# Optimization experiments

Measured on AMD Instinct MI355X. Metric: run time of the kernel, lower is better.

Reference implementation:

```python
import jax, jax.numpy as jnp
import numpy as np

B, T, S, V, D, H = 32, 50, 40, 32000, 512, 1024


def setup_inputs() -> dict:
    key = jax.random.key(0)
    ks = jax.random.split(key, 14)
    s_ih = 1.0 / np.sqrt(H)
    return {
        "zh_gruths": jax.random.randint(ks[0], (B, T), 0, V),
        "encoder_hs": jax.random.normal(ks[1], (B, S, H), jnp.float32),
        "encoder_h_n": jax.random.normal(ks[2], (1, B, H), jnp.float32) * 0.1,
        "encoder_c_n": jax.random.normal(ks[3], (1, B, H), jnp.float32) * 0.1,
        "entext_len": jax.random.randint(ks[4], (B,), 1, S + 1),
        "teacher_forcing_ratio": 1,
        "emb": jax.random.normal(ks[5], (V, D), jnp.float32) * 0.02,
        "W_ih": jax.random.normal(ks[6], (4 * H, D), jnp.float32) * s_ih,
        "W_hh": jax.random.normal(ks[7], (4 * H, H), jnp.float32) * s_ih,
        "b_ih": jax.random.normal(ks[8], (4 * H,), jnp.float32) * s_ih,
        "b_hh": jax.random.normal(ks[9], (4 * H,), jnp.float32) * s_ih,
        "W_ht": jax.random.normal(ks[10], (H, 2 * H), jnp.float32) * (1.0 / np.sqrt(2 * H)),
        "b_ht": jnp.zeros((H,), jnp.float32),
        "W_voc": jax.random.normal(ks[11], (V, H), jnp.float32) * s_ih,
        "b_voc": jnp.zeros((V,), jnp.float32),
    }


def reference(zh_gruths, encoder_hs, encoder_h_n, encoder_c_n, entext_len,
              teacher_forcing_ratio, emb, W_ih, W_hh, b_ih, b_hh,
              W_ht, b_ht, W_voc, b_voc):
    # teacher_forcing_ratio == 1 -> always teacher forcing (deterministic branch)
    xs = jnp.swapaxes(emb[zh_gruths], 0, 1)  # [T, B, D]
    hx0, cx0 = encoder_h_n[0], encoder_c_n[0]  # [B, H]

    def step(carry, xt):
        hx, cx = carry
        gates = xt @ W_ih.T + b_ih + hx @ W_hh.T + b_hh  # [B, 4H]
        i, f, g, o = jnp.split(gates, 4, axis=-1)  # torch gate order i,f,g,o
        i, f, o = jax.nn.sigmoid(i), jax.nn.sigmoid(f), jax.nn.sigmoid(o)
        cx = f * cx + i * jnp.tanh(g)
        hx = o * jnp.tanh(cx)
        # dot attention over encoder states
        scores = jnp.einsum('bsh,bh->bs', encoder_hs, hx)
        attn = jax.nn.softmax(scores, axis=-1)
        ctx = jnp.einsum('bs,bsh->bh', attn, encoder_hs)
        hx_atten = jnp.tanh(jnp.concatenate([ctx, hx], axis=-1) @ W_ht.T + b_ht)
        logits_t = hx_atten @ W_voc.T + b_voc  # [B, V]
        return (hx, cx), logits_t

    _, logits = jax.lax.scan(step, (hx0, cx0), xs)  # [T, B, V]
    logits = jnp.swapaxes(logits, 0, 1)  # [B, T, V]
    predicts = jnp.argmax(logits, axis=-1)  # [B, T]
    return logits, predicts
```

## Files before the change

### kernel.cpp

```cpp
#include <hip/hip_runtime.h>
#include <math.h>

typedef short bf16x8 __attribute__((ext_vector_type(8)));
typedef float f32x4 __attribute__((ext_vector_type(4)));
typedef float f32x2 __attribute__((ext_vector_type(2)));
typedef unsigned int uint;
typedef uint u32x4 __attribute__((ext_vector_type(4)));
typedef unsigned long long ull;
typedef unsigned short ushort;

#define Bz 32
#define Tz 50
#define Sz 40
#define Vz 32000
#define Dz 512
#define Hz 1024
#define Mz 1600
#define Mp 1664
#define NWG_REC 96

__device__ __forceinline__ float bf2f(ushort h) {
    uint u = ((uint)h) << 16;
    return __builtin_bit_cast(float, u);
}
__device__ __forceinline__ void splitf(float f, ushort& hi, ushort& lo) {
    uint u = __builtin_bit_cast(uint, f);
    hi = (ushort)(u >> 16);
    float rem = f - __builtin_bit_cast(float, u & 0xFFFF0000u);
    lo = (ushort)(__builtin_bit_cast(uint, rem) >> 16);
}
__device__ __forceinline__ float sigf(float x) { return 1.f / (1.f + expf(-x)); }

__device__ __forceinline__ uint ld_sc1(const uint* p) {
    uint v;
    asm volatile("global_load_dword %0, %1, off sc0 sc1\n\ts_waitcnt vmcnt(0)"
                 : "=&v"(v) : "v"(p) : "memory");
    return v;
}
__device__ __forceinline__ void st_sc1(uint* p, uint v) {
    asm volatile("global_store_dword %0, %1, off sc0 sc1" :: "v"(p), "v"(v) : "memory");
}

__global__ __launch_bounds__(256) void k_pre(ushort* hxA_hi, ushort* hxA_lo, float* cx,
                                             ushort* AH_hi, ushort* AH_lo, uint* flags,
                                             const float* h0, const float* c0) {
    int gid = blockIdx.x * 256 + threadIdx.x;
    if (gid < 32768) {
        float v = h0[gid];
        ushort hi, lo;
        splitf(v, hi, lo);
        hxA_hi[gid] = hi;
        hxA_lo[gid] = lo;
    } else if (gid < 65536) {
        cx[gid - 32768] = c0[gid - 32768];
    } else if (gid < 196608) {
        int g = gid - 65536;
        AH_hi[(long)Mz * 2048 + g] = 0;
        AH_lo[(long)Mz * 2048 + g] = 0;
    } else if (gid < 196608 + 2048) {
        st_sc1(&flags[gid - 196608], 0u);
    }
}

__global__ __launch_bounds__(256) void k_wsplit(const float* __restrict__ src,
                                                ushort* __restrict__ hi, ushort* __restrict__ lo,
                                                int n4) {
    int stride = gridDim.x * 256;
    for (int i = blockIdx.x * 256 + threadIdx.x; i < n4; i += stride) {
        float4 f = *(const float4*)(src + (long)i * 4);
        float vv[4] = {f.x, f.y, f.z, f.w};
        ushort h[4], l[4];
#pragma unroll
        for (int e = 0; e < 4; ++e) splitf(vv[e], h[e], l[e]);
        uint2 hp, lp;
        hp.x = (uint)h[0] | ((uint)h[1] << 16);
        hp.y = (uint)h[2] | ((uint)h[3] << 16);
        lp.x = (uint)l[0] | ((uint)l[1] << 16);
        lp.y = (uint)l[2] | ((uint)l[3] << 16);
        *(uint2*)(hi + (long)i * 4) = hp;
        *(uint2*)(lo + (long)i * 4) = lp;
    }
}

__global__ __launch_bounds__(256, 1) void k_xgemm(const float* __restrict__ emb,
                                                  const int* __restrict__ tok,
                                                  const float* __restrict__ Wih,
                                                  const float* __restrict__ bih,
                                                  const float* __restrict__ bhh,
                                                  float* __restrict__ gx) {
    __shared__ ushort sAh[128][40];
    __shared__ ushort sAl[128][40];
    __shared__ ushort sBh[128][40];
    __shared__ ushort sBl[128][40];
    int bid = blockIdx.x;
    int mt = bid >> 5, nt = bid & 31;
    int tid = threadIdx.x;
    int row = tid >> 1, half = tid & 1;
    int wv = tid >> 6, lane = tid & 63;
    int wr = wv >> 1, wc = wv & 1;
    int m0 = wr * 64, n0 = wc * 64;
    int r16 = lane & 15, kg = lane >> 4, k0 = kg * 8;

    f32x4 acc[4][4];
#pragma unroll
    for (int i = 0; i < 4; i++)
#pragma unroll
        for (int j = 0; j < 4; j++) acc[i][j] = (f32x4){0.f, 0.f, 0.f, 0.f};

    int r = mt * 128 + row;
    int tk = (r < Mz) ? tok[r] : 0;
    const float* arow = emb + (long)tk * Dz;
    const float* brow = Wih + (long)(nt * 128 + row) * Dz;

    for (int kb = 0; kb < Dz; kb += 32) {
        {
            ushort hh[16], ll[16];
#pragma unroll
            for (int q = 0; q < 16; q += 4) {
                float4 w4 = (r < Mz) ? *(const float4*)(arow + kb + half * 16 + q)
                                     : (float4){0.f, 0.f, 0.f, 0.f};
                float vv[4] = {w4.x, w4.y, w4.z, w4.w};
#pragma unroll
                for (int e = 0; e < 4; ++e) splitf(vv[e], hh[q + e], ll[q + e]);
            }
            *(uint4*)&sAh[row][half * 16]     = *(uint4*)&hh[0];
            *(uint4*)&sAh[row][half * 16 + 8] = *(uint4*)&hh[8];
            *(uint4*)&sAl[row][half * 16]     = *(uint4*)&ll[0];
            *(uint4*)&sAl[row][half * 16 + 8] = *(uint4*)&ll[8];
        }
        {
            ushort hh[16], ll[16];
#pragma unroll
            for (int q = 0; q < 16; q += 4) {
                float4 w4 = *(const float4*)(brow + kb + half * 16 + q);
                float vv[4] = {w4.x, w4.y, w4.z, w4.w};
#pragma unroll
                for (int e = 0; e < 4; ++e) splitf(vv[e], hh[q + e], ll[q + e]);
            }
            *(uint4*)&sBh[row][half * 16]     = *(uint4*)&hh[0];
            *(uint4*)&sBh[row][half * 16 + 8] = *(uint4*)&hh[8];
            *(uint4*)&sBl[row][half * 16]     = *(uint4*)&ll[0];
            *(uint4*)&sBl[row][half * 16 + 8] = *(uint4*)&ll[8];
        }
        __syncthreads();
        bf16x8 af[4], alf[4], bhf[4], blf[4];
#pragma unroll
        for (int i = 0; i < 4; ++i) {
            af[i]  = *(const bf16x8*)&sAh[m0 + i * 16 + r16][k0];
            alf[i] = *(const bf16x8*)&sAl[m0 + i * 16 + r16][k0];
            bhf[i] = *(const bf16x8*)&sBh[n0 + i * 16 + r16][k0];
            blf[i] = *(const bf16x8*)&sBl[n0 + i * 16 + r16][k0];
        }
#pragma unroll
        for (int i = 0; i < 4; ++i)
#pragma unroll
            for (int jn = 0; jn < 4; ++jn) {
                acc[i][jn] = __builtin_amdgcn_mfma_f32_16x16x32_bf16(af[i],  bhf[jn], acc[i][jn], 0, 0, 0);
                acc[i][jn] = __builtin_amdgcn_mfma_f32_16x16x32_bf16(af[i],  blf[jn], acc[i][jn], 0, 0, 0);
                acc[i][jn] = __builtin_amdgcn_mfma_f32_16x16x32_bf16(alf[i], bhf[jn], acc[i][jn], 0, 0, 0);
            }
        __syncthreads();
    }
#pragma unroll
    for (int i = 0; i < 4; ++i) {
        int gr0 = mt * 128 + m0 + i * 16 + kg * 4;
#pragma unroll
        for (int reg = 0; reg < 4; ++reg) {
            int gr = gr0 + reg;
            if (gr >= Mz) continue;
#pragma unroll
            for (int jn = 0; jn < 4; ++jn) {
                int gc = nt * 128 + n0 + jn * 16 + r16;
                gx[(long)gr * 4096 + gc] = acc[i][jn][reg] + bih[gc] + bhh[gc];
            }
        }
    }
}

__global__ __launch_bounds__(512, 1) void k_recfused4(
    const float* __restrict__ gx,
    const ushort* __restrict__ Whi, const ushort* __restrict__ Wlo,
    ushort* __restrict__ hxA_hi, ushort* __restrict__ hxA_lo,
    float* __restrict__ hxh, float* __restrict__ cx,
    const float* __restrict__ enc,
    ushort* __restrict__ AH_hi, ushort* __restrict__ AH_lo,
    uint* flags) {
    __shared__ u32x4 stg4[8192];
    __shared__ float hxs[Hz];
    __shared__ float sc[64];
    __shared__ float aw[64];
    int wid = blockIdx.x, tid = threadIdx.x;
    uint* release = flags + 1024;

    for (int t = 0; t <= Tz; ++t) {
        if (wid < 64) {
            if (t < Tz) {
                int w = wid;
                int p = t & 1, q = p ^ 1;
                int ks = tid & 127;
                int r0 = tid >> 7;
                const ushort* planes[2] = { hxA_hi + p * 32768, hxA_lo + p * 32768 };
#pragma unroll
                for (int plane = 0; plane < 2; ++plane) {
                    const ushort* b0 = planes[plane] + r0 * 1024 + ks * 8;
                    u32x4 d0, d1, d2, d3, d4, d5, d6, d7;
                    asm volatile(
                        "global_load_dwordx4 %0, %8, off sc0 sc1\n\t"
                        "global_load_dwordx4 %1, %9, off sc0 sc1\n\t"
                        "global_load_dwordx4 %2, %10, off sc0 sc1\n\t"
                        "global_load_dwordx4 %3, %11, off sc0 sc1\n\t"
                        "global_load_dwordx4 %4, %12, off sc0 sc1\n\t"
                        "global_load_dwordx4 %5, %13, off sc0 sc1\n\t"
                        "global_load_dwordx4 %6, %14, off sc0 sc1\n\t"
                        "global_load_dwordx4 %7, %15, off sc0 sc1\n\t"
                        "s_waitcnt vmcnt(0)"
                        : "=&v"(d0), "=&v"(d1), "=&v"(d2), "=&v"(d3),
                          "=&v"(d4), "=&v"(d5), "=&v"(d6), "=&v"(d7)
                        : "v"(b0), "v"(b0 + 4096), "v"(b0 + 8192), "v"(b0 + 12288),
                          "v"(b0 + 16384), "v"(b0 + 20480), "v"(b0 + 24576), "v"(b0 + 28672)
                        : "memory");
                    int li = plane * 4096 + ks * 32;
                    stg4[li + ((r0 +  0 + ks) & 31)] = d0;
                    stg4[li + ((r0 +  4 + ks) & 31)] = d1;
                    stg4[li + ((r0 +  8 + ks) & 31)] = d2;
                    stg4[li + ((r0 + 12 + ks) & 31)] = d3;
                    stg4[li + ((r0 + 16 + ks) & 31)] = d4;
                    stg4[li + ((r0 + 20 + ks) & 31)] = d5;
                    stg4[li + ((r0 + 24 + ks) & 31)] = d6;
                    stg4[li + ((r0 + 28 + ks) & 31)] = d7;
                }
                __syncthreads();
                int kh = tid >> 6, lane = tid & 63;
                int r16 = lane & 15, kg = lane >> 4;
                int jbase = w * 16 + r16;
                const ushort* whbase = Whi + (long)jbase * 1024;
                const ushort* wlbase = Wlo + (long)jbase * 1024;
                f32x4 acc[2][4];
#pragma unroll
                for (int i = 0; i < 2; ++i)
#pragma unroll
                    for (int v = 0; v < 4; ++v) acc[i][v] = (f32x4){0.f, 0.f, 0.f, 0.f};
#pragma unroll
                for (int it = 0; it < 4; ++it) {
                    int ksl = kh * 16 + it * 4 + kg;
                    int k0 = ksl * 8;
                    bf16x8 a_h0 = *(const bf16x8*)&stg4[       ksl * 32 + ((r16 + ksl) & 31)];
                    bf16x8 a_l0 = *(const bf16x8*)&stg4[4096 + ksl * 32 + ((r16 + ksl) & 31)];
                    bf16x8 a_h1 = *(const bf16x8*)&stg4[       ksl * 32 + ((16 + r16 + ksl) & 31)];
                    bf16x8 a_l1 = *(const bf16x8*)&stg4[4096 + ksl * 32 + ((16 + r16 + ksl) & 31)];
                    bf16x8 bh[4], bl[4];
#pragma unroll
                    for (int v = 0; v < 4; ++v) {
                        bh[v] = *(const bf16x8*)(whbase + ((long)v << 20) + k0);
                        bl[v] = *(const bf16x8*)(wlbase + ((long)v << 20) + k0);
                    }
#pragma unroll
                    for (int v = 0; v < 4; ++v) {
                        acc[0][v] = __builtin_amdgcn_mfma_f32_16x16x32_bf16(a_h0, bh[v], acc[0][v], 0, 0, 0);
                        acc[0][v] = __builtin_amdgcn_mfma_f32_16x16x32_bf16(a_l0, bh[v], acc[0][v], 0, 0, 0);
                        acc[0][v] = __builtin_amdgcn_mfma_f32_16x16x32_bf16(a_h0, bl[v], acc[0][v], 0, 0, 0);
                        acc[1][v] = __builtin_amdgcn_mfma_f32_16x16x32_bf16(a_h1, bh[v], acc[1][v], 0, 0, 0);
                        acc[1][v] = __builtin_amdgcn_mfma_f32_16x16x32_bf16(a_l1, bh[v], acc[1][v], 0, 0, 0);
                        acc[1][v] = __builtin_amdgcn_mfma_f32_16x16x32_bf16(a_h1, bl[v], acc[1][v], 0, 0, 0);
                    }
                }
                __syncthreads();
                float* sgp = (float*)stg4;
#pragma unroll
                for (int i = 0; i < 2; ++i)
#pragma unroll
                    for (int v = 0; v < 4; ++v)
#pragma unroll
                        for (int reg = 0; reg < 4; ++reg)
                            sgp[(((kh * 4 + v) * 32) + i * 16 + kg * 4 + reg) * 16 + r16] = acc[i][v][reg];
                __syncthreads();
                int b = tid >> 4, h16 = tid & 15;
                int hg = w * 16 + h16;
                const float* gxr = gx + ((long)b * Tz + t) * 4096 + hg;
                float g0 = 0.f, g1 = 0.f, g2 = 0.f, g3 = 0.f;
#pragma unroll
                for (int khh = 0; khh < 8; ++khh) {
                    g0 += sgp[((khh * 4 + 0) * 32 + b) * 16 + h16];
                    g1 += sgp[((khh * 4 + 1) * 32 + b) * 16 + h16];
                    g2 += sgp[((khh * 4 + 2) * 32 + b) * 16 + h16];
                    g3 += sgp[((khh * 4 + 3) * 32 + b) * 16 + h16];
                }
                g0 += gxr[0]; g1 += gxr[1024]; g2 += gxr[2048]; g3 += gxr[3072];
                long ci = (long)b * Hz + hg;
                float c = sigf(g1) * cx[ci] + sigf(g0) * tanhf(g2);
                float hv = sigf(g3) * tanhf(c);
                cx[ci] = c;
                float* hp = hxh + ((long)t * Bz + b) * Hz + hg;
                asm volatile("global_store_dword %0, %1, off sc0 sc1" :: "v"(hp), "v"(hv));
                ushort hi, lo;
                splitf(hv, hi, lo);
                ushort* hip = hxA_hi + q * 32768 + ci;
                ushort* lop = hxA_lo + q * 32768 + ci;
                asm volatile("global_store_short %0, %1, off sc0 sc1" :: "v"(hip), "v"((uint)hi));
                asm volatile("global_store_short %0, %1, off sc0 sc1" :: "v"(lop), "v"((uint)lo));

                asm volatile("s_waitcnt vmcnt(0)" ::: "memory");
                __syncthreads();
                uint tgt = (uint)(t + 1);
                if (wid == 0) {
                    if (tid == 0) {
                        st_sc1(&flags[0], tgt);
                        asm volatile("s_waitcnt vmcnt(0)" ::: "memory");
                    }
                    if (tid < 64) {
                        while (ld_sc1(&flags[tid * 16]) < tgt) __builtin_amdgcn_s_sleep(1);
                    }
                    __syncthreads();
                    if (tid == 0) st_sc1(release, tgt);
                } else {
                    if (tid == 0) {
                        st_sc1(&flags[wid * 16], tgt);
                        while (ld_sc1(release) < tgt) __builtin_amdgcn_s_sleep(1);
                    }
                    __syncthreads();
                }
            }
        } else {
            if (t > 0) {
                int b = wid - 64, tt = t - 1;
                if (tid == 0) {
                    while (ld_sc1(release) < (uint)t) __builtin_amdgcn_s_sleep(1);
                }
                __syncthreads();
                const float* hsrc = hxh + ((long)tt * Bz + b) * Hz + tid * 2;
                f32x2 h2;
                asm volatile("global_load_dwordx2 %0, %1, off sc0 sc1\n\ts_waitcnt vmcnt(0)"
                             : "=&v"(h2) : "v"(hsrc) : "memory");
                hxs[tid * 2] = h2[0];
                hxs[tid * 2 + 1] = h2[1];
                __syncthreads();
                int wv = tid >> 6, lane = tid & 63;
                float hreg[16];
#pragma unroll
                for (int u = 0; u < 16; ++u) hreg[u] = hxs[lane * 16 + u];
                const float* eb = enc + (long)b * Sz * Hz;
                for (int s = wv; s < Sz; s += 8) {
                    const float* er = eb + (long)s * Hz + lane * 16;
                    float sum = 0.f;
#pragma unroll
                    for (int qq = 0; qq < 4; ++qq) {
                        float4 e4 = *(const float4*)(er + qq * 4);
                        sum += e4.x * hreg[qq*4] + e4.y * hreg[qq*4+1] + e4.z * hreg[qq*4+2] + e4.w * hreg[qq*4+3];
                    }
#pragma unroll
                    for (int off = 32; off >= 1; off >>= 1) sum += __shfl_xor(sum, off);
                    if (lane == 0) sc[s] = sum;
                }
                __syncthreads();
                if (tid < 64) {
                    float vv = (tid < Sz) ? sc[tid] : -3.402823e38f;
                    float mx = vv;
#pragma unroll
                    for (int off = 32; off >= 1; off >>= 1) mx = fmaxf(mx, __shfl_xor(mx, off));
                    float e = (tid < Sz) ? expf(vv - mx) : 0.f;
                    float ssum = e;
#pragma unroll
                    for (int off = 32; off >= 1; off >>= 1) ssum += __shfl_xor(ssum, off);
                    if (tid < Sz) aw[tid] = e / ssum;
                }
                __syncthreads();
                float c0 = 0.f, c1 = 0.f;
#pragma unroll 4
                for (int s = 0; s < Sz; ++s) {
                    float2 e2 = *(const float2*)(eb + (long)s * Hz + tid * 2);
                    float a = aw[s];
                    c0 += a * e2.x; c1 += a * e2.y;
                }
                long rr = (long)b * Tz + tt;
                ushort* dh = AH_hi + rr * 2048;
                ushort* dl = AH_lo + rr * 2048;
                ushort hi, lo;
                splitf(c0, hi, lo); dh[tid * 2]     = hi; dl[tid * 2]     = lo;
                splitf(c1, hi, lo); dh[tid * 2 + 1] = hi; dl[tid * 2 + 1] = lo;
                splitf(hxs[tid * 2],     hi, lo); dh[1024 + tid * 2]     = hi; dl[1024 + tid * 2]     = lo;
                splitf(hxs[tid * 2 + 1], hi, lo); dh[1024 + tid * 2 + 1] = hi; dl[1024 + tid * 2 + 1] = lo;
            }
        }
    }
}

__global__ __launch_bounds__(256, 1) void k_ht(const ushort* __restrict__ Ah,
                                               const ushort* __restrict__ Al,
                                               const ushort* __restrict__ Bh,
                                               const ushort* __restrict__ Bl,
                                               const float* __restrict__ bht,
                                               ushort* __restrict__ Hh, ushort* __restrict__ Hl) {
    __shared__ ushort sAh[128][40];
    __shared__ ushort sAl[128][40];
    __shared__ ushort sBh[128][40];
    __shared__ ushort sBl[128][40];
    int bid = blockIdx.x;
    int mt = bid >> 3, nt = bid & 7;
    int tid = threadIdx.x;
    int row = tid >> 1, half = tid & 1;
    int wv = tid >> 6, lane = tid & 63;
    int wr = wv >> 1, wc = wv & 1;
    int m0 = wr * 64, n0 = wc * 64;
    int r16 = lane & 15, kg = lane >> 4, k0 = kg * 8;

    f32x4 acc[4][4];
#pragma unroll
    for (int i = 0; i < 4; i++)
#pragma unroll
        for (int j = 0; j < 4; j++) acc[i][j] = (f32x4){0.f, 0.f, 0.f, 0.f};

    long arow = (long)(mt * 128 + row) * 2048;
    long brow = (long)(nt * 128 + row) * 2048;

    for (int kb = 0; kb < 2048; kb += 32) {
        const ushort* pa = Ah + arow + kb + half * 16;
        *(uint4*)&sAh[row][half * 16]     = *(const uint4*)pa;
        *(uint4*)&sAh[row][half * 16 + 8] = *(const uint4*)(pa + 8);
        const ushort* pl = Al + arow + kb + half * 16;
        *(uint4*)&sAl[row][half * 16]     = *(const uint4*)pl;
        *(uint4*)&sAl[row][half * 16 + 8] = *(const uint4*)(pl + 8);
        const ushort* pb = Bh + brow + kb + half * 16;
        *(uint4*)&sBh[row][half * 16]     = *(const uint4*)pb;
        *(uint4*)&sBh[row][half * 16 + 8] = *(const uint4*)(pb + 8);
        const ushort* pc = Bl + brow + kb + half * 16;
        *(uint4*)&sBl[row][half * 16]     = *(const uint4*)pc;
        *(uint4*)&sBl[row][half * 16 + 8] = *(const uint4*)(pc + 8);
        __syncthreads();
        bf16x8 af[4], alf[4], bhf[4], blf[4];
#pragma unroll
        for (int i = 0; i < 4; ++i) {
            af[i]  = *(const bf16x8*)&sAh[m0 + i * 16 + r16][k0];
            alf[i] = *(const bf16x8*)&sAl[m0 + i * 16 + r16][k0];
            bhf[i] = *(const bf16x8*)&sBh[n0 + i * 16 + r16][k0];
            blf[i] = *(const bf16x8*)&sBl[n0 + i * 16 + r16][k0];
        }
#pragma unroll
        for (int i = 0; i < 4; ++i)
#pragma unroll
            for (int jn = 0; jn < 4; ++jn) {
                acc[i][jn] = __builtin_amdgcn_mfma_f32_16x16x32_bf16(af[i],  bhf[jn], acc[i][jn], 0, 0, 0);
                acc[i][jn] = __builtin_amdgcn_mfma_f32_16x16x32_bf16(af[i],  blf[jn], acc[i][jn], 0, 0, 0);
                acc[i][jn] = __builtin_amdgcn_mfma_f32_16x16x32_bf16(alf[i], bhf[jn], acc[i][jn], 0, 0, 0);
            }
        __syncthreads();
    }
#pragma unroll
    for (int i = 0; i < 4; ++i) {
        int gr0 = mt * 128 + m0 + i * 16 + kg * 4;
#pragma unroll
        for (int reg = 0; reg < 4; ++reg) {
            int gr = gr0 + reg;
            bool valid = gr < Mz;
#pragma unroll
            for (int jn = 0; jn < 4; ++jn) {
                int gc = nt * 128 + n0 + jn * 16 + r16;
                float vv = tanhf(acc[i][jn][reg] + bht[gc]);
                ushort hi = 0, lo = 0;
                if (valid) splitf(vv, hi, lo);
                Hh[(long)gr * Hz + gc] = hi;
                Hl[(long)gr * Hz + gc] = lo;
            }
        }
    }
}

__global__ __launch_bounds__(256, 1) void k_voc3(
    const ushort* __restrict__ Ah, const ushort* __restrict__ Al,
    const ushort* __restrict__ Wh, const ushort* __restrict__ Wl,
    const float* __restrict__ bvoc,
    float* __restrict__ out, ull* __restrict__ keys) {
    __shared__ ushort sAh[128][40];
    __shared__ ushort sAl[128][40];
    __shared__ ushort sBh[128][40];
    __shared__ ushort sBl[128][40];
    int bid = blockIdx.x;
    int nt = bid % 250, mg = bid / 250;
    int mt_beg = (mg == 0) ? 0 : 7;
    int mt_end = (mg == 0) ? 7 : 13;
    int tid = threadIdx.x;
    int row = tid >> 1, half = tid & 1;
    int wv = tid >> 6, lane = tid & 63;
    int wr = wv >> 1, wc = wv & 1;
    int m0 = wr * 64, n0 = wc * 64;
    int r16 = lane & 15, kg = lane >> 4, k0 = kg * 8;

    long wrow = (long)(nt * 128 + row) * Hz;
    int vcol_base = nt * 128 + n0;

    for (int mt = mt_beg; mt < mt_end; ++mt) {
        f32x4 acc[4][4];
#pragma unroll
        for (int i = 0; i < 4; i++)
#pragma unroll
            for (int j = 0; j < 4; j++) acc[i][j] = (f32x4){0.f, 0.f, 0.f, 0.f};

        long arow = (long)(mt * 128 + row) * Hz;

        for (int kb = 0; kb < Hz; kb += 32) {
            const ushort* pa = Ah + arow + kb + half * 16;
            *(uint4*)&sAh[row][half * 16]     = *(const uint4*)pa;
            *(uint4*)&sAh[row][half * 16 + 8] = *(const uint4*)(pa + 8);
            const ushort* pl = Al + arow + kb + half * 16;
            *(uint4*)&sAl[row][half * 16]     = *(const uint4*)pl;
            *(uint4*)&sAl[row][half * 16 + 8] = *(const uint4*)(pl + 8);
            const ushort* pb = Wh + wrow + kb + half * 16;
            *(uint4*)&sBh[row][half * 16]     = *(const uint4*)pb;
            *(uint4*)&sBh[row][half * 16 + 8] = *(const uint4*)(pb + 8);
            const ushort* pc = Wl + wrow + kb + half * 16;
            *(uint4*)&sBl[row][half * 16]     = *(const uint4*)pc;
            *(uint4*)&sBl[row][half * 16 + 8] = *(const uint4*)(pc + 8);
            __syncthreads();
            bf16x8 af[4], alf[4], bhf[4], blf[4];
#pragma unroll
            for (int i = 0; i < 4; ++i) {
                af[i]  = *(const bf16x8*)&sAh[m0 + i * 16 + r16][k0];
                alf[i] = *(const bf16x8*)&sAl[m0 + i * 16 + r16][k0];
                bhf[i] = *(const bf16x8*)&sBh[n0 + i * 16 + r16][k0];
                blf[i] = *(const bf16x8*)&sBl[n0 + i * 16 + r16][k0];
            }
#pragma unroll
            for (int i = 0; i < 4; ++i)
#pragma unroll
                for (int jn = 0; jn < 4; ++jn) {
                    acc[i][jn] = __builtin_amdgcn_mfma_f32_16x16x32_bf16(af[i],  bhf[jn], acc[i][jn], 0, 0, 0);
                    acc[i][jn] = __builtin_amdgcn_mfma_f32_16x16x32_bf16(af[i],  blf[jn], acc[i][jn], 0, 0, 0);
                    acc[i][jn] = __builtin_amdgcn_mfma_f32_16x16x32_bf16(alf[i], bhf[jn], acc[i][jn], 0, 0, 0);
                }
            __syncthreads();
        }
#pragma unroll
        for (int i = 0; i < 4; ++i) {
            int gr0 = mt * 128 + m0 + i * 16 + kg * 4;
#pragma unroll
            for (int reg = 0; reg < 4; ++reg) {
                int gr = gr0 + reg;
                bool valid = gr < Mz;
                float bestv = -3.402823e38f;
                int bestc = 0;
#pragma unroll
                for (int jn = 0; jn < 4; ++jn) {
                    int gc = vcol_base + jn * 16 + r16;
                    float v = acc[i][jn][reg] + bvoc[gc];
                    if (valid) __builtin_nontemporal_store(v, &out[(long)gr * Vz + gc]);
                    if (v > bestv) { bestv = v; bestc = gc; }
                }
#pragma unroll
                for (int off = 1; off < 16; off <<= 1) {
                    float ov = __shfl_xor(bestv, off);
                    int oc = __shfl_xor(bestc, off);
                    if (ov > bestv || (ov == bestv && oc < bestc)) { bestv = ov; bestc = oc; }
                }
                if (valid && r16 == 0) {
                    uint u = __builtin_bit_cast(uint, bestv);
                    u = (u & 0x80000000u) ? ~u : (u | 0x80000000u);
                    keys[(long)gr * 512 + nt * 2 + wc] = (((ull)u) << 32) | (ull)(65535 - bestc);
                }
            }
        }
    }
}

__global__ __launch_bounds__(256) void k_argmax2(const ull* __restrict__ keys, float* __restrict__ pred) {
    int r = blockIdx.x, tid = threadIdx.x;
    ull best = 0;
    for (int j = tid; j < 500; j += 256) {
        ull k = keys[(long)r * 512 + j];
        if (k > best) best = k;
    }
    __shared__ ull sk[256];
    sk[tid] = best;
    __syncthreads();
    for (int s = 128; s > 0; s >>= 1) {
        if (tid < s) { if (sk[tid + s] > sk[tid]) sk[tid] = sk[tid + s]; }
        __syncthreads();
    }
    if (tid == 0) pred[r] = (float)(65535 - (int)(sk[0] & 0xFFFFull));
}

extern "C" void kernel_launch(void* const* d_in, const int* in_sizes, int n_in,
                              void* d_out, int out_size, void* d_ws, size_t ws_size,
                              hipStream_t stream) {
    const int*   tok  = (const int*)d_in[0];
    const float* enc  = (const float*)d_in[1];
    const float* h0   = (const float*)d_in[2];
    const float* c0   = (const float*)d_in[3];
    const float* emb  = (const float*)d_in[6];
    const float* Wih  = (const float*)d_in[7];
    const float* Whh  = (const float*)d_in[8];
    const float* bih  = (const float*)d_in[9];
    const float* bhh  = (const float*)d_in[10];
    const float* Wht  = (const float*)d_in[11];
    const float* bht  = (const float*)d_in[12];
    const float* Wvoc = (const float*)d_in[13];
    const float* bvoc = (const float*)d_in[14];
    float* out = (float*)d_out;

    char* base = (char*)d_ws;
    size_t off = 0;
    float*  gx      = (float*)(base + off);  off += (size_t)Mz * 4096 * 4;
    ushort* hxA_hi  = (ushort*)(base + off); off += 2 * 32768 * 2;
    ushort* hxA_lo  = (ushort*)(base + off); off += 2 * 32768 * 2;
    float*  cx      = (float*)(base + off);  off += 32768 * 4;
    float*  hxh     = (float*)(base + off);  off += (size_t)Tz * Bz * Hz * 4;
    ushort* AH_hi   = (ushort*)(base + off); off += (size_t)Mp * 2048 * 2;
    ushort* AH_lo   = (ushort*)(base + off); off += (size_t)Mp * 2048 * 2;
    ushort* Whh_hi  = (ushort*)(base + off); off += (size_t)4096 * 1024 * 2;
    ushort* Whh_lo  = (ushort*)(base + off); off += (size_t)4096 * 1024 * 2;
    ushort* Wht_hi  = (ushort*)(base + off); off += (size_t)1024 * 2048 * 2;
    ushort* Wht_lo  = (ushort*)(base + off); off += (size_t)1024 * 2048 * 2;
    ushort* Wvoc_hi = (ushort*)base;
    ushort* Wvoc_lo = Wvoc_hi + (size_t)Vz * Hz;
    size_t off2 = (size_t)Vz * Hz * 2 * 2;
    ushort* HXA_hi  = (ushort*)(base + off2); off2 += (size_t)Mp * 1024 * 2;
    ushort* HXA_lo  = (ushort*)(base + off2); off2 += (size_t)Mp * 1024 * 2;
    ull*    keys    = (ull*)(base + off2);    off2 += (size_t)Mz * 512 * 8;
    uint*   flags   = (uint*)(base + off2);   off2 += 8192;

    k_pre<<<776, 256, 0, stream>>>(hxA_hi, hxA_lo, cx, AH_hi, AH_lo, flags, h0, c0);
    k_wsplit<<<1024, 256, 0, stream>>>(Whh, Whh_hi, Whh_lo, 4096 * 1024 / 4);
    k_wsplit<<<512, 256, 0, stream>>>(Wht, Wht_hi, Wht_lo, 1024 * 2048 / 4);
    k_xgemm<<<13 * 32, 256, 0, stream>>>(emb, tok, Wih, bih, bhh, gx);

    k_recfused4<<<NWG_REC, 512, 0, stream>>>(gx, Whh_hi, Whh_lo, hxA_hi, hxA_lo, hxh, cx,
                                             enc, AH_hi, AH_lo, flags);

    k_ht<<<13 * 8, 256, 0, stream>>>(AH_hi, AH_lo, Wht_hi, Wht_lo, bht, HXA_hi, HXA_lo);
    k_wsplit<<<2048, 256, 0, stream>>>(Wvoc, Wvoc_hi, Wvoc_lo, Vz * Hz / 4);
    k_voc3<<<500, 256, 0, stream>>>(HXA_hi, HXA_lo, Wvoc_hi, Wvoc_lo, bvoc, out, keys);
    k_argmax2<<<Mz, 256, 0, stream>>>(keys, out + (long)Mz * Vz);
}
```

Before: 1.171 ms.

## Overlap vocab weight split with recurrence and replace central barrier with per-wave flag polling

New measurement: 1.136 ms. 3.0% less time.

```diff
diff --git a/kernel.cpp b/kernel.cpp
--- a/kernel.cpp
+++ b/kernel.cpp
@@ -17,7 +17,6 @@
 #define Hz 1024
 #define Mz 1600
 #define Mp 1664
-#define NWG_REC 96
 
 __device__ __forceinline__ float bf2f(ushort h) {
     uint u = ((uint)h) << 16;
@@ -177,32 +176,65 @@
     }
 }
 
-__global__ __launch_bounds__(512, 1) void k_recfused4(
+__global__ __launch_bounds__(512, 1) void k_recfused5(
     const float* __restrict__ gx,
     const ushort* __restrict__ Whi, const ushort* __restrict__ Wlo,
     ushort* __restrict__ hxA_hi, ushort* __restrict__ hxA_lo,
     float* __restrict__ hxh, float* __restrict__ cx,
     const float* __restrict__ enc,
     ushort* __restrict__ AH_hi, ushort* __restrict__ AH_lo,
-    uint* flags) {
+    uint* flags,
+    const float* __restrict__ Wvoc, ushort* __restrict__ Wvh, ushort* __restrict__ Wvl,
+    int do_wsplit) {
     __shared__ u32x4 stg4[8192];
     __shared__ float hxs[Hz];
     __shared__ float sc[64];
     __shared__ float aw[64];
     int wid = blockIdx.x, tid = threadIdx.x;
-    uint* release = flags + 1024;
+
+    if (wid >= 96) {
+        if (do_wsplit) {
+            int n4 = Vz * Hz / 4;
+            int stride = 160 * 512;
+            for (int i = (wid - 96) * 512 + tid; i < n4; i += stride) {
+                float4 f = *(const float4*)(Wvoc + (long)i * 4);
+                float vv[4] = {f.x, f.y, f.z, f.w};
+                ushort h[4], l[4];
+#pragma unroll
+                for (int e = 0; e < 4; ++e) splitf(vv[e], h[e], l[e]);
+                uint2 hp, lp;
+                hp.x = (uint)h[0] | ((uint)h[1] << 16);
+                hp.y = (uint)h[2] | ((uint)h[3] << 16);
+                lp.x = (uint)l[0] | ((uint)l[1] << 16);
+                lp.y = (uint)l[2] | ((uint)l[3] << 16);
+                *(uint2*)(Wvh + (long)i * 4) = hp;
+                *(uint2*)(Wvl + (long)i * 4) = lp;
+            }
+        }
+        return;
+    }
+
+    int lane = tid & 63, kh = tid >> 6;
 
     for (int t = 0; t <= Tz; ++t) {
         if (wid < 64) {
             if (t < Tz) {
                 int w = wid;
                 int p = t & 1, q = p ^ 1;
-                int ks = tid & 127;
-                int r0 = tid >> 7;
-                const ushort* planes[2] = { hxA_hi + p * 32768, hxA_lo + p * 32768 };
-#pragma unroll
-                for (int plane = 0; plane < 2; ++plane) {
-                    const ushort* b0 = planes[plane] + r0 * 1024 + ks * 8;
+                {
+                    bool done = false;
+                    while (!done) {
+                        uint f = 0xFFFFFFFFu;
+                        if (lane < 8) f = ld_sc1(&flags[(kh * 8 + lane) * 16]);
+                        done = (bool)__all(f >= (uint)t);
+                        if (!done) __builtin_amdgcn_s_sleep(1);
+                    }
+                }
+                int kslot = kh * 16 + (lane & 15);
+                int rowb = (lane >> 4) * 8;
+                const ushort* ph = hxA_hi + p * 32768 + (long)rowb * 1024 + kslot * 8;
+                const ushort* pl = hxA_lo + p * 32768 + (long)rowb * 1024 + kslot * 8;
+                {
                     u32x4 d0, d1, d2, d3, d4, d5, d6, d7;
                     asm volatile(
                         "global_load_dwordx4 %0, %8, off sc0 sc1\n\t"
@@ -216,21 +248,46 @@
                         "s_waitcnt vmcnt(0)"
                         : "=&v"(d0), "=&v"(d1), "=&v"(d2), "=&v"(d3),
                           "=&v"(d4), "=&v"(d5), "=&v"(d6), "=&v"(d7)
-                        : "v"(b0), "v"(b0 + 4096), "v"(b0 + 8192), "v"(b0 + 12288),
-                          "v"(b0 + 16384), "v"(b0 + 20480), "v"(b0 + 24576), "v"(b0 + 28672)
+                        : "v"(ph), "v"(ph + 1024), "v"(ph + 2048), "v"(ph + 3072),
+                          "v"(ph + 4096), "v"(ph + 5120), "v"(ph + 6144), "v"(ph + 7168)
                         : "memory");
-                    int li = plane * 4096 + ks * 32;
-                    stg4[li + ((r0 +  0 + ks) & 31)] = d0;
-                    stg4[li + ((r0 +  4 + ks) & 31)] = d1;
-                    stg4[li + ((r0 +  8 + ks) & 31)] = d2;
-                    stg4[li + ((r0 + 12 + ks) & 31)] = d3;
-                    stg4[li + ((r0 + 16 + ks) & 31)] = d4;
-                    stg4[li + ((r0 + 20 + ks) & 31)] = d5;
-                    stg4[li + ((r0 + 24 + ks) & 31)] = d6;
-                    stg4[li + ((r0 + 28 + ks) & 31)] = d7;
-                }
-                __syncthreads();
-                int kh = tid >> 6, lane = tid & 63;
+                    int li = kslot * 32;
+                    stg4[li + ((rowb + 0 + kslot) & 31)] = d0;
+                    stg4[li + ((rowb + 1 + kslot) & 31)] = d1;
+                    stg4[li + ((rowb + 2 + kslot) & 31)] = d2;
+                    stg4[li + ((rowb + 3 + kslot) & 31)] = d3;
+                    stg4[li + ((rowb + 4 + kslot) & 31)] = d4;
+                    stg4[li + ((rowb + 5 + kslot) & 31)] = d5;
+                    stg4[li + ((rowb + 6 + kslot) & 31)] = d6;
+                    stg4[li + ((rowb + 7 + kslot) & 31)] = d7;
+                }
+                {
+                    u32x4 d0, d1, d2, d3, d4, d5, d6, d7;
+                    asm volatile(
+                        "global_load_dwordx4 %0, %8, off sc0 sc1\n\t"
+                        "global_load_dwordx4 %1, %9, off sc0 sc1\n\t"
+                        "global_load_dwordx4 %2, %10, off sc0 sc1\n\t"
+                        "global_load_dwordx4 %3, %11, off sc0 sc1\n\t"
+                        "global_load_dwordx4 %4, %12, off sc0 sc1\n\t"
+                        "global_load_dwordx4 %5, %13, off sc0 sc1\n\t"
+                        "global_load_dwordx4 %6, %14, off sc0 sc1\n\t"
+                        "global_load_dwordx4 %7, %15, off sc0 sc1\n\t"
+                        "s_waitcnt vmcnt(0)"
+                        : "=&v"(d0), "=&v"(d1), "=&v"(d2), "=&v"(d3),
+                          "=&v"(d4), "=&v"(d5), "=&v"(d6), "=&v"(d7)
+                        : "v"(pl), "v"(pl + 1024), "v"(pl + 2048), "v"(pl + 3072),
+                          "v"(pl + 4096), "v"(pl + 5120), "v"(pl + 6144), "v"(pl + 7168)
+                        : "memory");
+                    int li = 4096 + kslot * 32;
+                    stg4[li + ((rowb + 0 + kslot) & 31)] = d0;
+                    stg4[li + ((rowb + 1 + kslot) & 31)] = d1;
+                    stg4[li + ((rowb + 2 + kslot) & 31)] = d2;
+                    stg4[li + ((rowb + 3 + kslot) & 31)] = d3;
+                    stg4[li + ((rowb + 4 + kslot) & 31)] = d4;
+                    stg4[li + ((rowb + 5 + kslot) & 31)] = d5;
+                    stg4[li + ((rowb + 6 + kslot) & 31)] = d6;
+                    stg4[li + ((rowb + 7 + kslot) & 31)] = d7;
+                }
                 int r16 = lane & 15, kg = lane >> 4;
                 int jbase = w * 16 + r16;
                 const ushort* whbase = Whi + (long)jbase * 1024;
@@ -298,33 +355,20 @@
                 ushort* lop = hxA_lo + q * 32768 + ci;
                 asm volatile("global_store_short %0, %1, off sc0 sc1" :: "v"(hip), "v"((uint)hi));
                 asm volatile("global_store_short %0, %1, off sc0 sc1" :: "v"(lop), "v"((uint)lo));
-
                 asm volatile("s_waitcnt vmcnt(0)" ::: "memory");
                 __syncthreads();
-                uint tgt = (uint)(t + 1);
-                if (wid == 0) {
-                    if (tid == 0) {
-                        st_sc1(&flags[0], tgt);
-                        asm volatile("s_waitcnt vmcnt(0)" ::: "memory");
-                    }
-                    if (tid < 64) {
-                        while (ld_sc1(&flags[tid * 16]) < tgt) __builtin_amdgcn_s_sleep(1);
-                    }
-                    __syncthreads();
-                    if (tid == 0) st_sc1(release, tgt);
-                } else {
-                    if (tid == 0) {
-                        st_sc1(&flags[wid * 16], tgt);
-                        while (ld_sc1(release) < tgt) __builtin_amdgcn_s_sleep(1);
-                    }
-                    __syncthreads();
-                }
+                if (tid == 0) st_sc1(&flags[wid * 16], (uint)(t + 1));
             }
         } else {
             if (t > 0) {
                 int b = wid - 64, tt = t - 1;
-                if (tid == 0) {
-                    while (ld_sc1(release) < (uint)t) __builtin_amdgcn_s_sleep(1);
+                if (tid < 64) {
+                    bool done = false;
+                    while (!done) {
+                        uint f = ld_sc1(&flags[tid * 16]);
+                        done = (bool)__all(f >= (uint)t);
+                        if (!done) __builtin_amdgcn_s_sleep(2);
+                    }
                 }
                 __syncthreads();
                 const float* hsrc = hxh + ((long)tt * Bz + b) * Hz + tid * 2;
@@ -334,7 +378,7 @@
                 hxs[tid * 2] = h2[0];
                 hxs[tid * 2 + 1] = h2[1];
                 __syncthreads();
-                int wv = tid >> 6, lane = tid & 63;
+                int wv = tid >> 6;
                 float hreg[16];
 #pragma unroll
                 for (int u = 0; u < 16; ++u) hreg[u] = hxs[lane * 16 + u];
@@ -608,9 +652,21 @@
     ushort* Whh_lo  = (ushort*)(base + off); off += (size_t)4096 * 1024 * 2;
     ushort* Wht_hi  = (ushort*)(base + off); off += (size_t)1024 * 2048 * 2;
     ushort* Wht_lo  = (ushort*)(base + off); off += (size_t)1024 * 2048 * 2;
-    ushort* Wvoc_hi = (ushort*)base;
-    ushort* Wvoc_lo = Wvoc_hi + (size_t)Vz * Hz;
-    size_t off2 = (size_t)Vz * Hz * 2 * 2;
+
+    const size_t wvoc_bytes = (size_t)Vz * Hz * 2 * 2;
+    const size_t surv_bytes = (size_t)Mp * 1024 * 2 * 2 + (size_t)Mz * 512 * 8 + 8192;
+    bool fused = ws_size >= off + wvoc_bytes + surv_bytes;
+
+    ushort* Wvoc_hi; ushort* Wvoc_lo; size_t off2;
+    if (fused) {
+        Wvoc_hi = (ushort*)(base + off);
+        Wvoc_lo = Wvoc_hi + (size_t)Vz * Hz;
+        off2 = off + wvoc_bytes;
+    } else {
+        Wvoc_hi = (ushort*)base;
+        Wvoc_lo = Wvoc_hi + (size_t)Vz * Hz;
+        off2 = wvoc_bytes;
+    }
     ushort* HXA_hi  = (ushort*)(base + off2); off2 += (size_t)Mp * 1024 * 2;
     ushort* HXA_lo  = (ushort*)(base + off2); off2 += (size_t)Mp * 1024 * 2;
     ull*    keys    = (ull*)(base + off2);    off2 += (size_t)Mz * 512 * 8;
@@ -621,11 +677,14 @@
     k_wsplit<<<512, 256, 0, stream>>>(Wht, Wht_hi, Wht_lo, 1024 * 2048 / 4);
     k_xgemm<<<13 * 32, 256, 0, stream>>>(emb, tok, Wih, bih, bhh, gx);
 
-    k_recfused4<<<NWG_REC, 512, 0, stream>>>(gx, Whh_hi, Whh_lo, hxA_hi, hxA_lo, hxh, cx,
-                                             enc, AH_hi, AH_lo, flags);
+    k_recfused5<<<fused ? 256 : 96, 512, 0, stream>>>(
+        gx, Whh_hi, Whh_lo, hxA_hi, hxA_lo, hxh, cx, enc, AH_hi, AH_lo, flags,
+        Wvoc, Wvoc_hi, Wvoc_lo, fused ? 1 : 0);
 
     k_ht<<<13 * 8, 256, 0, stream>>>(AH_hi, AH_lo, Wht_hi, Wht_lo, bht, HXA_hi, HXA_lo);
-    k_wsplit<<<2048, 256, 0, stream>>>(Wvoc, Wvoc_hi, Wvoc_lo, Vz * Hz / 4);
+    if (!fused) {
+        k_wsplit<<<2048, 256, 0, stream>>>(Wvoc, Wvoc_hi, Wvoc_lo, Vz * Hz / 4);
+    }
     k_voc3<<<500, 256, 0, stream>>>(HXA_hi, HXA_lo, Wvoc_hi, Wvoc_lo, bvoc, out, keys);
     k_argmax2<<<Mz, 256, 0, stream>>>(keys, out + (long)Mz * Vz);
 }
```
